# Kernel tuning notes

Measured on AMD Instinct MI355X. Metric: run time of the kernel, lower is better.

Reference implementation:

```python
import jax, jax.numpy as jnp
import numpy as np

NUM_HEADS = 16
EPS = 1e-5


def _layernorm(x, w):
    # torch LayerNorm (biased variance), bias=False
    m = jnp.mean(x, axis=-1, keepdims=True)
    v = jnp.mean(jnp.square(x - m), axis=-1, keepdims=True)
    return (x - m) * jax.lax.rsqrt(v + EPS) * w


def setup_inputs() -> dict:
    key = jax.random.key(0)
    ks = jax.random.split(key, 8)
    B, S, H, A = 2, 2048, 1024, 1024
    hd = H // NUM_HEADS
    return {
        "x": jax.random.normal(ks[0], (B, S, H), jnp.float32),
        "ada_cond": jax.random.normal(ks[1], (B, A), jnp.float32),
        "freqs": jax.random.normal(ks[2], (S, hd // 2, 2), jnp.float32),
        "w_qkv": jax.random.normal(ks[3], (3 * H, H), jnp.float32) * (1.0 / np.sqrt(H)),
        "w_o": jax.random.normal(ks[4], (H, H), jnp.float32) * (1.0 / np.sqrt(H)),
        "ln_w": jnp.ones((H,), jnp.float32),
        "mod_w": jax.random.normal(ks[5], (3 * H, A), jnp.float32) * 0.02,
        "mod_b": jax.random.normal(ks[6], (3 * H,), jnp.float32) * 0.02,
        "qn_w": jnp.ones((hd,), jnp.float32),
        "kn_w": jnp.ones((hd,), jnp.float32),
    }


def reference(x, ada_cond, freqs, w_qkv, w_o, ln_w, mod_w, mod_b, qn_w, kn_w):
    B, S, H = x.shape
    nh = NUM_HEADS
    hd = H // nh

    # pre-norm + AdaLN modulation (with gate)
    h = _layernorm(x, ln_w)
    mod = (jax.nn.silu(ada_cond) @ mod_w.T + mod_b)[:, None, :]  # [B,1,3H]
    scale, shift, gate = jnp.split(mod, 3, axis=-1)
    h = h * (scale + 1.0) + shift

    # QKV projection and head split
    qkv = h @ w_qkv.T                                  # [B,S,3H]
    q, k, v = jnp.split(qkv, 3, axis=-1)
    to_heads = lambda t: t.reshape(B, S, nh, hd).transpose(0, 2, 1, 3)  # [B,nh,S,hd]
    q, k, v = to_heads(q), to_heads(k), to_heads(v)

    # per-head QK layernorm
    q = _layernorm(q, qn_w)
    k = _layernorm(k, kn_w)

    # RoPE (complex rotation via interleaved pairs)
    f = freqs[:S].reshape(1, 1, S, hd // 2, 2)

    def rope(t):
        tr = t.reshape(B, nh, S, hd // 2, 2)
        re = tr[..., 0] * f[..., 0] - tr[..., 1] * f[..., 1]
        im = tr[..., 1] * f[..., 0] + tr[..., 0] * f[..., 1]
        return jnp.stack([re, im], axis=-1).reshape(B, nh, S, hd)

    q, k = rope(q), rope(k)

    # scaled dot-product attention (non-causal)
    scores = jnp.einsum("bhqd,bhkd->bhqk", q, k) * (1.0 / np.sqrt(hd))
    attn = jax.nn.softmax(scores, axis=-1)
    o = jnp.einsum("bhqk,bhkd->bhqd", attn, v)
    o = o.transpose(0, 2, 1, 3).reshape(B, S, H)

    return (o @ w_o.T) * gate
```

## Files before the change

### kernel.cpp

```cpp
#include <hip/hip_runtime.h>
#include <hip/hip_bf16.h>
#include <math.h>

#define B_ 2
#define S_ 2048
#define H_ 1024
#define A_ 1024
#define NH_ 16
#define HD_ 64
#define H3_ 3072
#define EPS_ 1e-5f

typedef __attribute__((ext_vector_type(8))) short short8;
typedef __attribute__((ext_vector_type(4))) float floatx4;

__device__ inline unsigned short f2bf(float x) {
    union { float f; unsigned u; } v; v.f = x;
    unsigned r = v.u + 0x7fffu + ((v.u >> 16) & 1u);
    return (unsigned short)(r >> 16);
}

__device__ inline float bf2f(unsigned short u) {
    union { unsigned u; float f; } v; v.u = ((unsigned)u) << 16;
    return v.f;
}

__device__ inline unsigned pk_bf16(float a, float b) {
    union { __hip_bfloat162 h; unsigned u; } v;
    v.h = __float22bfloat162_rn(make_float2(a, b));
    return v.u;
}

__device__ inline void gld_lds16(const void* g, void* l) {
    __builtin_amdgcn_global_load_lds(
        (const __attribute__((address_space(1))) unsigned int*)g,
        (__attribute__((address_space(3))) unsigned int*)l, 16, 0, 0);
}

#define TBLK(r) ((((r) >> 3) * 544) + (((r) & 7) * 64))

__global__ __launch_bounds__(256) void cast_bf16_kernel(
    const float* __restrict__ in, unsigned short* __restrict__ out, int n)
{
    int i = (blockIdx.x * 256 + threadIdx.x) * 8;
    if (i >= n) return;
    float4 a = *(const float4*)(in + i);
    float4 b = *(const float4*)(in + i + 4);
    uint4 o;
    o.x = pk_bf16(a.x, a.y);
    o.y = pk_bf16(a.z, a.w);
    o.z = pk_bf16(b.x, b.y);
    o.w = pk_bf16(b.z, b.w);
    *(uint4*)(out + i) = o;
}

__global__ __launch_bounds__(256) void mod_gemv_kernel(
    const float* __restrict__ ada, const float* __restrict__ mod_w,
    const float* __restrict__ mod_b, float* __restrict__ mod)
{
    int wid = threadIdx.x >> 6;
    int lane = threadIdx.x & 63;
    int idx = blockIdx.x * 4 + wid;
    int b = idx / H3_;
    int j = idx % H3_;
    const float* ar = ada + (size_t)b * A_;
    const float* wr = mod_w + (size_t)j * A_;
    float acc = 0.f;
    for (int a = lane; a < A_; a += 64) {
        float av = ar[a];
        float sv = av / (1.f + __expf(-av));
        acc += sv * wr[a];
    }
    #pragma unroll
    for (int m = 1; m < 64; m <<= 1) acc += __shfl_xor(acc, m);
    if (lane == 0) mod[idx] = acc + mod_b[j];
}

__global__ __launch_bounds__(256) void ln_mod_kernel(
    const float* __restrict__ x, const float* __restrict__ ln_w,
    const float* __restrict__ mod, unsigned short* __restrict__ hout)
{
    int row = blockIdx.x;
    int b = row >> 11;
    const float* xr = x + (size_t)row * H_;
    int t = threadIdx.x;
    float4 xv = *(const float4*)(xr + t * 4);
    float s1 = xv.x + xv.y + xv.z + xv.w;
    float s2 = xv.x*xv.x + xv.y*xv.y + xv.z*xv.z + xv.w*xv.w;
    #pragma unroll
    for (int m = 1; m < 64; m <<= 1) { s1 += __shfl_xor(s1, m); s2 += __shfl_xor(s2, m); }
    __shared__ float r1[4], r2[4];
    int wid = t >> 6, lane = t & 63;
    if (lane == 0) { r1[wid] = s1; r2[wid] = s2; }
    __syncthreads();
    s1 = r1[0] + r1[1] + r1[2] + r1[3];
    s2 = r2[0] + r2[1] + r2[2] + r2[3];
    float mean = s1 * (1.f / H_);
    float var  = s2 * (1.f / H_) - mean * mean;
    float rstd = rsqrtf(var + EPS_);
    const float* mrow = mod + (size_t)b * H3_;
    float4 wv = *(const float4*)(ln_w + t * 4);
    float4 sc = *(const float4*)(mrow + t * 4);
    float4 sh = *(const float4*)(mrow + H_ + t * 4);
    float4 hv;
    hv.x = (xv.x - mean) * rstd * wv.x * (sc.x + 1.f) + sh.x;
    hv.y = (xv.y - mean) * rstd * wv.y * (sc.y + 1.f) + sh.y;
    hv.z = (xv.z - mean) * rstd * wv.z * (sc.z + 1.f) + sh.z;
    hv.w = (xv.w - mean) * rstd * wv.w * (sc.w + 1.f) + sh.w;
    uint2 o;
    o.x = pk_bf16(hv.x, hv.y);
    o.y = pk_bf16(hv.z, hv.w);
    *(uint2*)(hout + (size_t)row * H_ + t * 4) = o;
}

__global__ __launch_bounds__(256) void gemm_bt_bf16_kernel(
    const unsigned short* __restrict__ A, const unsigned short* __restrict__ Bm,
    void* __restrict__ C, int M, int N, int K, int out_bf16,
    const float* __restrict__ gate, int gate_stride, int batch_shift)
{
    __shared__ unsigned short As[128 * 32];
    __shared__ unsigned short Bs[128 * 32];
    int t = threadIdx.x;
    int w = t >> 6, lane = t & 63;
    int q16 = lane & 15, quad = lane >> 4;
    int wm = w >> 1, wn = w & 1;
    int m0 = blockIdx.y * 128, n0 = blockIdx.x * 128;

    int srow = (w << 5) + (lane >> 2);
    int soff = (lane & 3) << 3;
    const unsigned short* ga = A + (size_t)(m0 + srow) * K + soff;
    const unsigned short* gb = Bm + (size_t)(n0 + srow) * K + soff;
    unsigned short* la0 = As + (w << 5) * 32;
    unsigned short* la1 = la0 + 16 * 32;
    unsigned short* lb0 = Bs + (w << 5) * 32;
    unsigned short* lb1 = lb0 + 16 * 32;

    floatx4 acc[4][4];
    #pragma unroll
    for (int mt = 0; mt < 4; ++mt)
        #pragma unroll
        for (int nt = 0; nt < 4; ++nt)
            acc[mt][nt] = (floatx4){0.f, 0.f, 0.f, 0.f};

    int a_row = wm * 64 + q16;
    int b_row = wn * 64 + q16;

    for (int kt = 0; kt < K; kt += 32) {
        __syncthreads();
        gld_lds16(ga, la0);
        gld_lds16(ga + (size_t)16 * K, la1);
        gld_lds16(gb, lb0);
        gld_lds16(gb + (size_t)16 * K, lb1);
        ga += 32; gb += 32;
        __syncthreads();

        short8 af[4], bf[4];
        #pragma unroll
        for (int mt = 0; mt < 4; ++mt)
            af[mt] = *(const short8*)&As[(a_row + mt * 16) * 32 + quad * 8];
        #pragma unroll
        for (int nt = 0; nt < 4; ++nt)
            bf[nt] = *(const short8*)&Bs[(b_row + nt * 16) * 32 + quad * 8];
        #pragma unroll
        for (int mt = 0; mt < 4; ++mt)
            #pragma unroll
            for (int nt = 0; nt < 4; ++nt)
                acc[mt][nt] = __builtin_amdgcn_mfma_f32_16x16x32_bf16(
                    af[mt], bf[nt], acc[mt][nt], 0, 0, 0);
    }

    #pragma unroll
    for (int mt = 0; mt < 4; ++mt) {
        #pragma unroll
        for (int i = 0; i < 4; ++i) {
            int m = m0 + wm * 64 + mt * 16 + quad * 4 + i;
            const float* grow = gate ? gate + (size_t)(m >> batch_shift) * gate_stride
                                     : nullptr;
            #pragma unroll
            for (int nt = 0; nt < 4; ++nt) {
                int n = n0 + wn * 64 + nt * 16 + q16;
                float v = acc[mt][nt][i];
                if (gate) v *= grow[n];
                if (out_bf16)
                    ((unsigned short*)C)[(size_t)m * N + n] =
                        (unsigned short)pk_bf16(v, 0.f);
                else
                    ((float*)C)[(size_t)m * N + n] = v;
            }
        }
    }
}

__global__ __launch_bounds__(256) void qk_ln_rope_kernel(
    const unsigned short* __restrict__ qkv, const float* __restrict__ freqs,
    const float* __restrict__ qn_w, const float* __restrict__ kn_w,
    unsigned short* __restrict__ qout, unsigned short* __restrict__ kout,
    unsigned short* __restrict__ vtout)
{
    __shared__ unsigned short vt_lds[64][72];
    int t = threadIdx.x;
    int w = t >> 6, lane = t & 63;
    int bh = blockIdx.x >> 5;
    int sblk = blockIdx.x & 31;
    int h = bh & (NH_ - 1);
    int b = bh >> 4;

    float qnw = qn_w[lane], knw = kn_w[lane];

    for (int it = 0; it < 16; ++it) {
        int s_local = w * 16 + it;
        int s = sblk * 64 + s_local;
        const unsigned short* base = qkv + ((size_t)(b * S_ + s)) * H3_;
        float qv = bf2f(base[h * HD_ + lane]);
        float kv = bf2f(base[H_ + h * HD_ + lane]);
        unsigned short vv = base[2 * H_ + h * HD_ + lane];

        float qs1 = qv, qs2 = qv * qv, ks1 = kv, ks2 = kv * kv;
        #pragma unroll
        for (int m = 1; m < 64; m <<= 1) {
            qs1 += __shfl_xor(qs1, m); qs2 += __shfl_xor(qs2, m);
            ks1 += __shfl_xor(ks1, m); ks2 += __shfl_xor(ks2, m);
        }
        float qm = qs1 * (1.f / 64), qvar = qs2 * (1.f / 64) - qm * qm;
        float km = ks1 * (1.f / 64), kvar = ks2 * (1.f / 64) - km * km;
        qv = (qv - qm) * rsqrtf(qvar + EPS_) * qnw;
        kv = (kv - km) * rsqrtf(kvar + EPS_) * knw;

        float f0 = freqs[(size_t)s * 64 + (lane >> 1) * 2 + 0];
        float f1 = freqs[(size_t)s * 64 + (lane >> 1) * 2 + 1];
        float qp = __shfl_xor(qv, 1);
        float kp = __shfl_xor(kv, 1);
        float qr = (lane & 1) ? (qv * f0 + qp * f1) : (qv * f0 - qp * f1);
        float kr = (lane & 1) ? (kv * f0 + kp * f1) : (kv * f0 - kp * f1);

        size_t o = ((size_t)bh * S_ + s) * HD_ + lane;
        qout[o] = f2bf(qr * 0.1803368801111244f);
        kout[o] = f2bf(kr);
        vt_lds[lane][s_local] = vv;
    }
    __syncthreads();
    for (int i = t; i < 512; i += 256) {
        int r = i >> 3, c8 = i & 7;
        *(uint4*)(vtout + ((size_t)bh * 64 + r) * S_ + sblk * 64 + c8 * 8) =
            *(const uint4*)&vt_lds[r][c8 * 8];
    }
}

__global__ __launch_bounds__(256) void attn_mfma_kernel(
    const unsigned short* __restrict__ q, const unsigned short* __restrict__ k,
    const unsigned short* __restrict__ vt, unsigned short* __restrict__ o)
{
    __shared__ unsigned short Ks[8 * 544];
    __shared__ unsigned short Vs[8 * 544];
    __shared__ unsigned short Ps[4][16][72];

    int t = threadIdx.x;
    int w = t >> 6, lane = t & 63;
    int q16 = lane & 15, quad = lane >> 4;
    int bh = blockIdx.y, b = bh >> 4, h = bh & 15;
    int s0 = blockIdx.x * 64;

    const unsigned short* qg = q + ((size_t)bh * S_ + s0) * HD_;
    gld_lds16(qg + (2 * w) * 512 + lane * 8, &Ks[(2 * w) * 544]);
    gld_lds16(qg + (2 * w + 1) * 512 + lane * 8, &Ks[(2 * w + 1) * 544]);
    __syncthreads();
    int qrow = TBLK(16 * w + q16);
    short8 qf0 = *(const short8*)&Ks[qrow + quad * 8];
    short8 qf1 = *(const short8*)&Ks[qrow + 32 + quad * 8];

    short8 ones8;
    #pragma unroll
    for (int i = 0; i < 8; ++i) ones8[i] = (short)0x3F80;

    floatx4 acc_o[4];
    floatx4 acc_l = (floatx4){0.f, 0.f, 0.f, 0.f};
    #pragma unroll
    for (int i = 0; i < 4; ++i) acc_o[i] = (floatx4){0.f, 0.f, 0.f, 0.f};

    const unsigned short* kg = k + (size_t)bh * S_ * HD_;
    const unsigned short* vg = vt + (size_t)bh * 64 * S_;
    int vsrc = (16 * w + (lane >> 3)) * S_ + (lane & 7) * 8;

    for (int kt = 0; kt < S_ / 64; ++kt) {
        __syncthreads();
        gld_lds16(kg + (2 * w) * 512 + lane * 8, &Ks[(2 * w) * 544]);
        gld_lds16(kg + (2 * w + 1) * 512 + lane * 8, &Ks[(2 * w + 1) * 544]);
        gld_lds16(vg + vsrc, &Vs[(2 * w) * 544]);
        gld_lds16(vg + vsrc + 8 * S_, &Vs[(2 * w + 1) * 544]);
        kg += 64 * HD_;
        vg += 64;
        __syncthreads();

        floatx4 sc[4];
        #pragma unroll
        for (int nk = 0; nk < 4; ++nk) sc[nk] = (floatx4){-12.f, -12.f, -12.f, -12.f};
        #pragma unroll
        for (int nk = 0; nk < 4; ++nk) {
            int krow = TBLK(16 * nk + q16);
            short8 kf0 = *(const short8*)&Ks[krow + quad * 8];
            short8 kf1 = *(const short8*)&Ks[krow + 32 + quad * 8];
            sc[nk] = __builtin_amdgcn_mfma_f32_16x16x32_bf16(kf0, qf0, sc[nk], 0, 0, 0);
            sc[nk] = __builtin_amdgcn_mfma_f32_16x16x32_bf16(kf1, qf1, sc[nk], 0, 0, 0);
        }

        #pragma unroll
        for (int nk = 0; nk < 4; ++nk) {
            float p0 = __builtin_amdgcn_exp2f(sc[nk][0]);
            float p1 = __builtin_amdgcn_exp2f(sc[nk][1]);
            float p2 = __builtin_amdgcn_exp2f(sc[nk][2]);
            float p3 = __builtin_amdgcn_exp2f(sc[nk][3]);
            uint2 pk;
            pk.x = pk_bf16(p0, p1);
            pk.y = pk_bf16(p2, p3);
            *(uint2*)&Ps[w][q16][16 * nk + quad * 4] = pk;
        }

        __asm__ __volatile__("" ::: "memory");

        #pragma unroll
        for (int ks = 0; ks < 2; ++ks) {
            short8 pf = *(const short8*)&Ps[w][q16][ks * 32 + quad * 8];
            acc_l = __builtin_amdgcn_mfma_f32_16x16x32_bf16(ones8, pf, acc_l, 0, 0, 0);
            #pragma unroll
            for (int nd = 0; nd < 4; ++nd) {
                short8 vf = *(const short8*)&Vs[TBLK(16 * nd + q16) + ks * 32 + quad * 8];
                acc_o[nd] = __builtin_amdgcn_mfma_f32_16x16x32_bf16(vf, pf, acc_o[nd], 0, 0, 0);
            }
        }
    }

    float inv = 1.f / acc_l[0];
    #pragma unroll
    for (int nd = 0; nd < 4; ++nd) {
        uint2 pk;
        pk.x = pk_bf16(acc_o[nd][0] * inv, acc_o[nd][1] * inv);
        pk.y = pk_bf16(acc_o[nd][2] * inv, acc_o[nd][3] * inv);
        *(uint2*)&Ps[w][q16][16 * nd + quad * 4] = pk;
    }
    __asm__ __volatile__("" ::: "memory");
    unsigned short* og = o + ((size_t)(b * S_ + s0 + 16 * w + q16)) * H_ + h * HD_;
    #pragma unroll
    for (int i = 0; i < 2; ++i) {
        int c = quad * 2 + i;
        *(short8*)(og + c * 8) = *(const short8*)&Ps[w][q16][c * 8];
    }
}

extern "C" void kernel_launch(void* const* d_in, const int* in_sizes, int n_in,
                              void* d_out, int out_size, void* d_ws, size_t ws_size,
                              hipStream_t stream)
{
    const float* x     = (const float*)d_in[0];
    const float* ada   = (const float*)d_in[1];
    const float* freqs = (const float*)d_in[2];
    const float* w_qkv = (const float*)d_in[3];
    const float* w_o   = (const float*)d_in[4];
    const float* ln_w  = (const float*)d_in[5];
    const float* mod_w = (const float*)d_in[6];
    const float* mod_b = (const float*)d_in[7];
    const float* qn_w  = (const float*)d_in[8];
    const float* kn_w  = (const float*)d_in[9];
    float* out = (float*)d_out;

    float* ws  = (float*)d_ws;
    float* mod = ws;
    unsigned short* qkvb  = (unsigned short*)(mod + 8192);
    unsigned short* hb    = qkvb + (size_t)B_ * S_ * H3_;
    unsigned short* qb    = hb + (size_t)B_ * S_ * H_;
    unsigned short* kb    = qb + (size_t)B_ * S_ * H_;
    unsigned short* vtb   = kb + (size_t)B_ * S_ * H_;
    unsigned short* ob    = vtb + (size_t)B_ * S_ * H_;
    unsigned short* wqkvb = ob + (size_t)B_ * S_ * H_;
    unsigned short* wob   = wqkvb + (size_t)H3_ * H_;

    cast_bf16_kernel<<<H3_ * H_ / (8 * 256), 256, 0, stream>>>(w_qkv, wqkvb, H3_ * H_);
    cast_bf16_kernel<<<H_ * H_ / (8 * 256), 256, 0, stream>>>(w_o, wob, H_ * H_);
    mod_gemv_kernel<<<B_ * H3_ / 4, 256, 0, stream>>>(ada, mod_w, mod_b, mod);
    ln_mod_kernel<<<B_ * S_, 256, 0, stream>>>(x, ln_w, mod, hb);
    gemm_bt_bf16_kernel<<<dim3(H3_ / 128, B_ * S_ / 128), 256, 0, stream>>>(
        hb, wqkvb, qkvb, B_ * S_, H3_, H_, 1, nullptr, 0, 0);
    qk_ln_rope_kernel<<<B_ * NH_ * S_ / 64, 256, 0, stream>>>(
        qkvb, freqs, qn_w, kn_w, qb, kb, vtb);
    attn_mfma_kernel<<<dim3(S_ / 64, B_ * NH_), 256, 0, stream>>>(qb, kb, vtb, ob);
    gemm_bt_bf16_kernel<<<dim3(H_ / 128, B_ * S_ / 128), 256, 0, stream>>>(
        ob, wob, out, B_ * S_, H_, H_, 0, mod + 2 * H_, H3_, 11);
}
```

Measured before the change: 275.7 us.

## Double-buffer K/V tiles in attention kernel to overlap loads with MFMA

Keeps two LDS buffers for the K and V tiles and issues the global-to-LDS loads for the next key block before computing on the current one. This removes one barrier per iteration and aims to hide global load latency behind the QK and PV MFMA work. The cost is double the K/V LDS footprint, which can lower occupancy. If the compiler inserts a full vmcnt wait before the LDS reads, the intended overlap may not happen.

```diff
diff --git a/kernel.cpp b/kernel.cpp
--- a/kernel.cpp
+++ b/kernel.cpp
@@ -250,8 +250,8 @@
     const unsigned short* __restrict__ q, const unsigned short* __restrict__ k,
     const unsigned short* __restrict__ vt, unsigned short* __restrict__ o)
 {
-    __shared__ unsigned short Ks[8 * 544];
-    __shared__ unsigned short Vs[8 * 544];
+    __shared__ unsigned short Ks[2][8 * 544];
+    __shared__ unsigned short Vs[2][8 * 544];
     __shared__ unsigned short Ps[4][16][72];
 
     int t = threadIdx.x;
@@ -261,12 +261,13 @@
     int s0 = blockIdx.x * 64;
 
     const unsigned short* qg = q + ((size_t)bh * S_ + s0) * HD_;
-    gld_lds16(qg + (2 * w) * 512 + lane * 8, &Ks[(2 * w) * 544]);
-    gld_lds16(qg + (2 * w + 1) * 512 + lane * 8, &Ks[(2 * w + 1) * 544]);
+    gld_lds16(qg + (2 * w) * 512 + lane * 8, &Ks[0][(2 * w) * 544]);
+    gld_lds16(qg + (2 * w + 1) * 512 + lane * 8, &Ks[0][(2 * w + 1) * 544]);
     __syncthreads();
     int qrow = TBLK(16 * w + q16);
-    short8 qf0 = *(const short8*)&Ks[qrow + quad * 8];
-    short8 qf1 = *(const short8*)&Ks[qrow + 32 + quad * 8];
+    short8 qf0 = *(const short8*)&Ks[0][qrow + quad * 8];
+    short8 qf1 = *(const short8*)&Ks[0][qrow + 32 + quad * 8];
+    __syncthreads();
 
     short8 ones8;
     #pragma unroll
@@ -280,16 +281,29 @@
     const unsigned short* kg = k + (size_t)bh * S_ * HD_;
     const unsigned short* vg = vt + (size_t)bh * 64 * S_;
     int vsrc = (16 * w + (lane >> 3)) * S_ + (lane & 7) * 8;
+    int ksrc0 = (2 * w) * 512 + lane * 8;
+    int ksrc1 = (2 * w + 1) * 512 + lane * 8;
+
+    gld_lds16(kg + ksrc0, &Ks[0][(2 * w) * 544]);
+    gld_lds16(kg + ksrc1, &Ks[0][(2 * w + 1) * 544]);
+    gld_lds16(vg + vsrc, &Vs[0][(2 * w) * 544]);
+    gld_lds16(vg + vsrc + 8 * S_, &Vs[0][(2 * w + 1) * 544]);
 
     for (int kt = 0; kt < S_ / 64; ++kt) {
+        int cur = kt & 1, nxt = cur ^ 1;
         __syncthreads();
-        gld_lds16(kg + (2 * w) * 512 + lane * 8, &Ks[(2 * w) * 544]);
-        gld_lds16(kg + (2 * w + 1) * 512 + lane * 8, &Ks[(2 * w + 1) * 544]);
-        gld_lds16(vg + vsrc, &Vs[(2 * w) * 544]);
-        gld_lds16(vg + vsrc + 8 * S_, &Vs[(2 * w + 1) * 544]);
-        kg += 64 * HD_;
-        vg += 64;
-        __syncthreads();
+
+        if (kt + 1 < S_ / 64) {
+            const unsigned short* kg2 = kg + (kt + 1) * (64 * HD_);
+            const unsigned short* vg2 = vg + (kt + 1) * 64;
+            gld_lds16(kg2 + ksrc0, &Ks[nxt][(2 * w) * 544]);
+            gld_lds16(kg2 + ksrc1, &Ks[nxt][(2 * w + 1) * 544]);
+            gld_lds16(vg2 + vsrc, &Vs[nxt][(2 * w) * 544]);
+            gld_lds16(vg2 + vsrc + 8 * S_, &Vs[nxt][(2 * w + 1) * 544]);
+        }
+
+        const unsigned short* ksb = Ks[cur];
+        const unsigned short* vsb = Vs[cur];
 
         floatx4 sc[4];
         #pragma unroll
@@ -297,8 +311,8 @@
         #pragma unroll
         for (int nk = 0; nk < 4; ++nk) {
             int krow = TBLK(16 * nk + q16);
-            short8 kf0 = *(const short8*)&Ks[krow + quad * 8];
-            short8 kf1 = *(const short8*)&Ks[krow + 32 + quad * 8];
+            short8 kf0 = *(const short8*)&ksb[krow + quad * 8];
+            short8 kf1 = *(const short8*)&ksb[krow + 32 + quad * 8];
             sc[nk] = __builtin_amdgcn_mfma_f32_16x16x32_bf16(kf0, qf0, sc[nk], 0, 0, 0);
             sc[nk] = __builtin_amdgcn_mfma_f32_16x16x32_bf16(kf1, qf1, sc[nk], 0, 0, 0);
         }
@@ -323,7 +337,7 @@
             acc_l = __builtin_amdgcn_mfma_f32_16x16x32_bf16(ones8, pf, acc_l, 0, 0, 0);
             #pragma unroll
             for (int nd = 0; nd < 4; ++nd) {
-                short8 vf = *(const short8*)&Vs[TBLK(16 * nd + q16) + ks * 32 + quad * 8];
+                short8 vf = *(const short8*)&vsb[TBLK(16 * nd + q16) + ks * 32 + quad * 8];
                 acc_o[nd] = __builtin_amdgcn_mfma_f32_16x16x32_bf16(vf, pf, acc_o[nd], 0, 0, 0);
             }
         }
```

Measured after the change: 291.3 us. +5.7%, slower.
